# Performance work log

Measured on AMD Instinct MI355X. Metric: run time of the kernel, lower is better.

The kernel has to match this reference:

```python
import jax, jax.numpy as jnp
import numpy as np

B, S, F, H = 4, 1024, 256, 8
SCALE = float(F) ** 0.5  # source MULTIPLIES logits by sqrt(f)


def setup_inputs() -> dict:
    key = jax.random.key(0)
    ks = jax.random.split(key, 5)
    # 0.02 init scale keeps sigmoid logits in a non-saturated range
    return {
        "q_input": jax.random.normal(ks[0], (B, S, F), dtype=jnp.float32),
        "Wq": jax.random.normal(ks[1], (F, F * H), dtype=jnp.float32) * 0.02,
        "Wk": jax.random.normal(ks[2], (F, F * H), dtype=jnp.float32) * 0.02,
        "Wv": jax.random.normal(ks[3], (F, F * H), dtype=jnp.float32) * 0.02,
        "Wo": jax.random.normal(ks[4], (F * H, F), dtype=jnp.float32) * 0.02,
    }


def reference(q_input, Wq, Wk, Wv, Wo):
    b, s, f = q_input.shape
    h = Wq.shape[1] // f
    # kv_input is None in source -> self-attention (kv = q_input)
    q = (q_input.reshape(b * s, f) @ Wq).reshape(b, s, f, h)
    k = (q_input.reshape(b * s, f) @ Wk).reshape(b, s, f, h)
    v = (q_input.reshape(b * s, f) @ Wv).reshape(b, s, f, h)
    qkt = jnp.einsum('bifh,bjfh->bijh', q, k)          # [b, i, j, h]
    attn = jax.nn.sigmoid(qkt * SCALE)                  # sigmoid, NOT softmax
    wv = jnp.einsum('bijh,bjfh->bifh', attn, v)         # [b, i, f, h]
    wv = wv.reshape(b * s, f * h)
    out = jax.nn.relu(wv @ Wo)                          # projection + ReLU
    return out.reshape(b, s, f)
```

## Files before the change

### kernel.cpp

```cpp
#include <hip/hip_runtime.h>
#include <math.h>

#define SQ 1024
#define FQ 256
#define FH 2048

typedef _Float16 f16;
typedef f16  f16x8 __attribute__((ext_vector_type(8)));
typedef float f32x4 __attribute__((ext_vector_type(4)));

#define GLOAD_LDS16(gp, lp) \
    __builtin_amdgcn_global_load_lds((const __attribute__((address_space(1))) void*)(gp), \
                                     (__attribute__((address_space(3))) void*)(lp), 16, 0, 0)

#define SIG16(s) __builtin_amdgcn_rcpf(1.0f + __builtin_amdgcn_exp2f(-23.083120654223414f * (s)))

__global__ __launch_bounds__(256) void prep_kernel(const float* __restrict__ x,
                                                   const float* __restrict__ Wq,
                                                   const float* __restrict__ Wk,
                                                   const float* __restrict__ Wv,
                                                   const float* __restrict__ Wo,
                                                   f16* __restrict__ xh,
                                                   f16* __restrict__ wqT,
                                                   f16* __restrict__ wkT,
                                                   f16* __restrict__ wvT,
                                                   f16* __restrict__ woT) {
    const int z = blockIdx.z;
    if (z == 4) {
        int id = (int)(blockIdx.x * 8 + blockIdx.y);
        int idx = (id * 256 + (int)threadIdx.x) * 8;
        float4 a = *(const float4*)(x + idx);
        float4 b = *(const float4*)(x + idx + 4);
        f16x8 v = {(f16)a.x, (f16)a.y, (f16)a.z, (f16)a.w,
                   (f16)b.x, (f16)b.y, (f16)b.z, (f16)b.w};
        *(f16x8*)(xh + idx) = v;
        return;
    }
    __shared__ f16 T[32][33];
    const int tx = threadIdx.x & 31, ty = threadIdx.x >> 5;
    if (z < 3) {
        const float* W = z == 0 ? Wq : (z == 1 ? Wk : Wv);
        f16* WT        = z == 0 ? wqT : (z == 1 ? wkT : wvT);
        const int n0 = blockIdx.x * 32, k0 = blockIdx.y * 32;
#pragma unroll
        for (int i = 0; i < 4; ++i)
            T[ty + i * 8][tx] = (f16)W[(size_t)(k0 + ty + i * 8) * FH + n0 + tx];
        __syncthreads();
#pragma unroll
        for (int i = 0; i < 4; ++i)
            WT[(size_t)(n0 + ty + i * 8) * FQ + k0 + tx] = T[tx][ty + i * 8];
    } else {
        const int n0 = (blockIdx.x >> 3) * 32;
        const int yy = (blockIdx.x & 7) * 8 + blockIdx.y;
        const int ft = yy >> 3, h = yy & 7;
#pragma unroll
        for (int i = 0; i < 4; ++i) {
            int fl = ty + i * 8;
            T[fl][tx] = (f16)Wo[(size_t)((ft * 32 + fl) * 8 + h) * FQ + n0 + tx];
        }
        __syncthreads();
#pragma unroll
        for (int i = 0; i < 4; ++i)
            woT[(size_t)(n0 + ty + i * 8) * FH + h * 256 + ft * 32 + tx] = T[tx][ty + i * 8];
    }
}

__device__ __forceinline__ void stage_sw64(const f16* __restrict__ G, int ldg,
                                           int row0, int c0, f16* S,
                                           int nrows, int w, int lane) {
    const int rsub = lane >> 3;
    const int g    = (lane & 7) ^ (rsub & 7);
#pragma unroll
    for (int rI = w; rI < (nrows >> 3); rI += 4) {
        GLOAD_LDS16(G + (size_t)(row0 + rI * 8 + rsub) * ldg + c0 + g * 8,
                    S + rI * 512);
    }
}

__device__ __forceinline__ void gemm128_sw(const f16* __restrict__ A, int lda,
                                           const f16* __restrict__ Bt, int ldb,
                                           int kbeg, int kend, f16* As, f16* Bs,
                                           f32x4 acc[4][4], int row0, int col0) {
    const int t = threadIdx.x, lane = t & 63, w = t >> 6;
    const int wr = w >> 1, wc = w & 1;
    const int lrow = lane & 15, quad = lane >> 4;
    for (int k0 = kbeg; k0 < kend; k0 += 64) {
        __syncthreads();
        stage_sw64(A, lda, row0, k0, As, 128, w, lane);
        stage_sw64(Bt, ldb, col0, k0, Bs, 128, w, lane);
        __syncthreads();
#pragma unroll
        for (int kk = 0; kk < 2; ++kk) {
            f16x8 af[4], bf[4];
#pragma unroll
            for (int i = 0; i < 4; ++i) {
                int r = wr * 64 + i * 16 + lrow;
                af[i] = *(const f16x8*)&As[r * 64 + (((kk * 4 + quad) ^ (r & 7)) << 3)];
            }
#pragma unroll
            for (int j = 0; j < 4; ++j) {
                int r = wc * 64 + j * 16 + lrow;
                bf[j] = *(const f16x8*)&Bs[r * 64 + (((kk * 4 + quad) ^ (r & 7)) << 3)];
            }
#pragma unroll
            for (int i = 0; i < 4; ++i)
#pragma unroll
                for (int j = 0; j < 4; ++j)
                    acc[i][j] = __builtin_amdgcn_mfma_f32_16x16x32_f16(af[i], bf[j], acc[i][j], 0, 0, 0);
        }
    }
}

__global__ __launch_bounds__(256) void proj_mfma(const f16* __restrict__ xh,
                                                 const f16* __restrict__ wqT,
                                                 const f16* __restrict__ wkT,
                                                 const f16* __restrict__ wvT,
                                                 f16* __restrict__ qb,
                                                 f16* __restrict__ kb,
                                                 f16* __restrict__ vb) {
    const int z = blockIdx.z;
    const f16* WT = z == 0 ? wqT : (z == 1 ? wkT : wvT);
    f16* O        = z == 0 ? qb  : (z == 1 ? kb  : vb);
    __shared__ f16 smem[17408];
    f16* As = smem;
    f16* Bs = smem + 8192;
    f32x4 acc[4][4] = {};
    const int row0 = blockIdx.y * 128, col0 = blockIdx.x * 128;
    gemm128_sw(xh, FQ, WT, FQ, 0, FQ, As, Bs, acc, row0, col0);

    __syncthreads();
    f16* Es = smem;
    const int lane = threadIdx.x & 63, w = threadIdx.x >> 6;
    const int wr = w >> 1, wc = w & 1;
    const int lrow = lane & 15, quad = lane >> 4;
    if (z != 2) {
#pragma unroll
        for (int i = 0; i < 4; ++i)
#pragma unroll
            for (int rr = 0; rr < 4; ++rr) {
                int rl = 64 * wr + 16 * i + 4 * quad + rr;
#pragma unroll
                for (int j = 0; j < 4; ++j) {
                    int cc = 64 * wc + 16 * j + lrow;
                    Es[rl * 136 + (cc & 7) * 16 + (cc >> 3)] = (f16)acc[i][j][rr];
                }
            }
        __syncthreads();
        const int f0 = col0 >> 3;
#pragma unroll
        for (int it = 0; it < 4; ++it) {
            int c = it * 256 + threadIdx.x;
            int row = c >> 3, hh = c & 7;
            int gr = row0 + row, bbb = gr >> 10, s = gr & 1023;
            f16x8 v0 = *(const f16x8*)&Es[row * 136 + hh * 16];
            f16x8 v1 = *(const f16x8*)&Es[row * 136 + hh * 16 + 8];
            f16* dst = O + ((size_t)(bbb * 8 + hh) * SQ + s) * FQ + f0;
            *(f16x8*)dst = v0;
            *(f16x8*)(dst + 8) = v1;
        }
    } else {
#pragma unroll
        for (int i = 0; i < 4; ++i)
#pragma unroll
            for (int rr = 0; rr < 4; ++rr) {
                int rl = 64 * wr + 16 * i + 4 * quad + rr;
#pragma unroll
                for (int j = 0; j < 4; ++j) {
                    int cc = 64 * wc + 16 * j + lrow;
                    Es[cc * 136 + rl] = (f16)acc[i][j][rr];
                }
            }
        __syncthreads();
        const int bbb = row0 >> 10, s0 = row0 & 1023;
#pragma unroll
        for (int it = 0; it < 8; ++it) {
            int c = it * 256 + threadIdx.x;
            int cc = c >> 4, sc = c & 15;
            int hh = cc & 7, f = (col0 >> 3) + (cc >> 3);
            f16x8 v = *(const f16x8*)&Es[cc * 136 + sc * 8];
            *(f16x8*)(O + ((size_t)(bbb * 8 + hh) * FQ + f) * SQ + s0 + sc * 8) = v;
        }
    }
}

__global__ __launch_bounds__(512, 2) void fused_attn(const f16* __restrict__ Qb,
                                                     const f16* __restrict__ Kb,
                                                     const f16* __restrict__ Vt,
                                                     f16* __restrict__ WV) {
    __shared__ f16 smem[75776];
    const int t = threadIdx.x, lane = t & 63, w = t >> 6;
    const int grp = w >> 2, wl = w & 3;
    const int lrow = lane & 15, quad = lane >> 4;
    f16* Pw = smem + 65536 + w * 1280;
    const int n = blockIdx.x;
    const int xcd = n & 7, rest = n >> 3;
    const int bh = xcd * 4 + (rest & 3);
    const int strip = rest >> 2;
    const int m0 = strip * 128;
    const int bb = bh >> 3, h = bh & 7;
    const f16* Qg = Qb + (size_t)bh * SQ * FQ;
    const f16* Kg = Kb + (size_t)bh * SQ * FQ;
    const f16* Vg = Vt + (size_t)bh * FQ * SQ;

    f16x8 qf[2][8];
#pragma unroll
    for (int mi = 0; mi < 2; ++mi)
#pragma unroll
        for (int ks = 0; ks < 8; ++ks)
            qf[mi][ks] = *(const f16x8*)(Qg + (size_t)(m0 + 32 * wl + 16 * mi + lrow) * FQ
                                             + ks * 32 + quad * 8);

    const int krs = lane >> 5;
    const int kgp = lane & 31;
    const int vrs = lane >> 2;
    const int vgp = lane & 3;

    if (grp == 0) {
#pragma unroll
        for (int kt = 0; kt < 2; ++kt)
#pragma unroll
            for (int i = 0; i < 4; ++i) {
                int rI = wl + i * 4;
                int r = rI * 2 + krs;
                GLOAD_LDS16(Kg + (size_t)(kt * 32 + r) * FQ + ((kgp ^ (r & 7)) << 3),
                            smem + kt * 8192 + rI * 512);
            }
    } else {
#pragma unroll
        for (int kt = 0; kt < 2; ++kt)
#pragma unroll
            for (int i = 0; i < 4; ++i) {
                int rI = wl + i * 4;
                int f = rI * 16 + vrs;
                GLOAD_LDS16(Vg + (size_t)f * SQ + kt * 32 + ((vgp ^ ((f >> 1) & 3)) << 3),
                            smem + 32768 + kt * 8192 + rI * 512);
            }
    }

    f32x4 acc_o[2][16] = {};

    for (int it = 0; it < 16; ++it) {
        const int p = it & 1;
        f16* KBc = smem + (p * 2 + grp) * 8192;
        f16* VBc = smem + 32768 + (p * 2 + grp) * 8192;
        __syncthreads();
        if (it < 15) {
            const int pn = p ^ 1;
            const int base = (it + 1) * 64;
            if (grp == 0) {
#pragma unroll
                for (int kt = 0; kt < 2; ++kt)
#pragma unroll
                    for (int i = 0; i < 4; ++i) {
                        int rI = wl + i * 4;
                        int r = rI * 2 + krs;
                        GLOAD_LDS16(Kg + (size_t)(base + kt * 32 + r) * FQ + ((kgp ^ (r & 7)) << 3),
                                    smem + (pn * 2 + kt) * 8192 + rI * 512);
                    }
            } else {
#pragma unroll
                for (int kt = 0; kt < 2; ++kt)
#pragma unroll
                    for (int i = 0; i < 4; ++i) {
                        int rI = wl + i * 4;
                        int f = rI * 16 + vrs;
                        GLOAD_LDS16(Vg + (size_t)f * SQ + base + kt * 32 + ((vgp ^ ((f >> 1) & 3)) << 3),
                                    smem + 32768 + (pn * 2 + kt) * 8192 + rI * 512);
                    }
            }
        }
        f32x4 acc_s[2][2] = {};
#pragma unroll
        for (int ks = 0; ks < 8; ++ks) {
            f16x8 bf[2];
#pragma unroll
            for (int nj = 0; nj < 2; ++nj) {
                int rk = 16 * nj + lrow;
                bf[nj] = *(const f16x8*)&KBc[rk * 256 + (((ks * 4 + quad) ^ (rk & 7)) << 3)];
            }
#pragma unroll
            for (int mi = 0; mi < 2; ++mi)
#pragma unroll
                for (int nj = 0; nj < 2; ++nj)
                    acc_s[mi][nj] = __builtin_amdgcn_mfma_f32_16x16x32_f16(
                        qf[mi][ks], bf[nj], acc_s[mi][nj], 0, 0, 0);
        }
#pragma unroll
        for (int mi = 0; mi < 2; ++mi)
#pragma unroll
            for (int nj = 0; nj < 2; ++nj)
#pragma unroll
                for (int rr = 0; rr < 4; ++rr)
                    Pw[(16 * mi + 4 * quad + rr) * 40 + 16 * nj + lrow] =
                        (f16)SIG16(acc_s[mi][nj][rr]);
        f16x8 ap[2];
#pragma unroll
        for (int mi = 0; mi < 2; ++mi)
            ap[mi] = *(const f16x8*)&Pw[(16 * mi + lrow) * 40 + quad * 8];
#pragma unroll
        for (int nj = 0; nj < 16; ++nj) {
            int f = 16 * nj + lrow;
            f16x8 bv = *(const f16x8*)&VBc[f * 32 + ((quad ^ ((f >> 1) & 3)) << 3)];
#pragma unroll
            for (int mi = 0; mi < 2; ++mi)
                acc_o[mi][nj] = __builtin_amdgcn_mfma_f32_16x16x32_f16(
                    ap[mi], bv, acc_o[mi][nj], 0, 0, 0);
        }
    }
    __syncthreads();
    float* Fb = (float*)(smem + 34816);
    f16* Es = smem;
#pragma unroll
    for (int mi = 0; mi < 2; ++mi) {
        if (grp == 1) {
#pragma unroll
            for (int nj = 0; nj < 16; ++nj)
                *(f32x4*)&Fb[((wl * 16 + nj) << 8) + lane * 4] = acc_o[mi][nj];
        }
        __syncthreads();
        if (grp == 0) {
#pragma unroll
            for (int nj = 0; nj < 16; ++nj) {
                f32x4 s = acc_o[mi][nj] +
                          *(const f32x4*)&Fb[((wl * 16 + nj) << 8) + lane * 4];
#pragma unroll
                for (int rr = 0; rr < 4; ++rr)
                    Es[(32 * wl + 16 * mi + 4 * quad + rr) * 264 + 16 * nj + lrow] =
                        (f16)s[rr];
            }
        }
        __syncthreads();
    }
#pragma unroll
    for (int it = 0; it < 8; ++it) {
        int c = it * 512 + t;
        int r = c >> 5, ck = c & 31;
        f16x8 v = *(const f16x8*)&Es[r * 264 + ck * 8];
        *(f16x8*)(WV + (size_t)(bb * SQ + m0 + r) * FH + h * 256 + ck * 8) = v;
    }
}

__global__ __launch_bounds__(256) void out_mfma8(const f16* __restrict__ WVm,
                                                 const f16* __restrict__ WoT,
                                                 float* __restrict__ PP) {
    __shared__ f16 smem[16384];
    f16* As = smem;
    f16* Bs = smem + 8192;
    f32x4 acc[4][4] = {};
    const int row0 = blockIdx.y * 128, col0 = blockIdx.x * 128;
    const int kbeg = blockIdx.z * 256;
    gemm128_sw(WVm, FH, WoT, FH, kbeg, kbeg + 256, As, Bs, acc, row0, col0);

    float* P = PP + (size_t)blockIdx.z * SQ * 4 * FQ;
    const int lane = threadIdx.x & 63, w = threadIdx.x >> 6;
    const int wr = w >> 1, wc = w & 1;
    const int lrow = lane & 15, quad = lane >> 4;
#pragma unroll
    for (int i = 0; i < 4; ++i)
#pragma unroll
        for (int rr = 0; rr < 4; ++rr) {
            int gr = row0 + wr * 64 + i * 16 + quad * 4 + rr;
#pragma unroll
            for (int j = 0; j < 4; ++j) {
                int gc = col0 + wc * 64 + j * 16 + lrow;
                P[(size_t)gr * FQ + gc] = acc[i][j][rr];
            }
        }
}

__global__ __launch_bounds__(256) void reduce_relu8(const float* __restrict__ PP,
                                                    float* __restrict__ O) {
    int idx = (blockIdx.x * 256 + threadIdx.x) * 4;
    f32x4 s = *(const f32x4*)(PP + idx);
#pragma unroll
    for (int z = 1; z < 8; ++z)
        s += *(const f32x4*)(PP + (size_t)z * 1048576 + idx);
    f32x4 r = {fmaxf(s.x, 0.f), fmaxf(s.y, 0.f), fmaxf(s.z, 0.f), fmaxf(s.w, 0.f)};
    *(f32x4*)(O + idx) = r;
}

extern "C" void kernel_launch(void* const* d_in, const int* in_sizes, int n_in,
                              void* d_out, int out_size, void* d_ws, size_t ws_size,
                              hipStream_t stream) {
    const float* x  = (const float*)d_in[0];
    const float* Wq = (const float*)d_in[1];
    const float* Wk = (const float*)d_in[2];
    const float* Wv = (const float*)d_in[3];
    const float* Wo = (const float*)d_in[4];
    float* out = (float*)d_out;

    f16* ws = (f16*)d_ws;
    f16* xh    = ws;
    f16* wqT   = xh    + 1048576;
    f16* wkT   = wqT   + 524288;
    f16* wvT   = wkT   + 524288;
    f16* woT   = wvT   + 524288;
    f16* qbuf  = woT   + 524288;
    f16* kbuf  = qbuf  + 8388608;
    f16* vbuf  = kbuf  + 8388608;
    f16* wvbuf = vbuf  + 8388608;
    float* pp  = (float*)qbuf;

    dim3 blk(256);
    prep_kernel<<<dim3(64, 8, 5), blk, 0, stream>>>(x, Wq, Wk, Wv, Wo,
                                                    xh, wqT, wkT, wvT, woT);

    proj_mfma<<<dim3(16, 32, 3), blk, 0, stream>>>(xh, wqT, wkT, wvT, qbuf, kbuf, vbuf);

    fused_attn<<<dim3(256), dim3(512), 0, stream>>>(qbuf, kbuf, vbuf, wvbuf);

    out_mfma8<<<dim3(2, 32, 8), blk, 0, stream>>>(wvbuf, woT, pp);
    reduce_relu8<<<dim3(1024), blk, 0, stream>>>(pp, out);
}
```

Measured before the change: 161.3 us.

## Keep sigmoid probabilities in registers via transposed QK^T MFMA layout

Swaps the MFMA operand order for the QK^T product so the score accumulator lands in the layout needed as the A operand of the PV product. This removes the per-warp LDS write/read round trip for the sigmoid probabilities. The PV product now uses 16x16x16 MFMAs with 4-wide V fragments, which doubles the MFMA instruction count and the number of V reads from LDS. It also raises wave priority with s_setprio around the PV loop.

Result: slower. 176.2 us (+9.2%).

```diff
diff --git a/kernel.cpp b/kernel.cpp
--- a/kernel.cpp
+++ b/kernel.cpp
@@ -7,6 +7,7 @@
 
 typedef _Float16 f16;
 typedef f16  f16x8 __attribute__((ext_vector_type(8)));
+typedef f16  f16x4 __attribute__((ext_vector_type(4)));
 typedef float f32x4 __attribute__((ext_vector_type(4)));
 
 #define GLOAD_LDS16(gp, lp) \
@@ -191,7 +192,6 @@
     const int t = threadIdx.x, lane = t & 63, w = t >> 6;
     const int grp = w >> 2, wl = w & 3;
     const int lrow = lane & 15, quad = lane >> 4;
-    f16* Pw = smem + 65536 + w * 1280;
     const int n = blockIdx.x;
     const int xcd = n & 7, rest = n >> 3;
     const int bh = xcd * 4 + (rest & 3);
@@ -279,33 +279,39 @@
                 bf[nj] = *(const f16x8*)&KBc[rk * 256 + (((ks * 4 + quad) ^ (rk & 7)) << 3)];
             }
 #pragma unroll
-            for (int mi = 0; mi < 2; ++mi)
-#pragma unroll
-                for (int nj = 0; nj < 2; ++nj)
-                    acc_s[mi][nj] = __builtin_amdgcn_mfma_f32_16x16x32_f16(
-                        qf[mi][ks], bf[nj], acc_s[mi][nj], 0, 0, 0);
-        }
-#pragma unroll
-        for (int mi = 0; mi < 2; ++mi)
-#pragma unroll
             for (int nj = 0; nj < 2; ++nj)
 #pragma unroll
+                for (int mi = 0; mi < 2; ++mi)
+                    acc_s[nj][mi] = __builtin_amdgcn_mfma_f32_16x16x32_f16(
+                        bf[nj], qf[mi][ks], acc_s[nj][mi], 0, 0, 0);
+        }
+        f16x4 ap[2][2];
+#pragma unroll
+        for (int nj = 0; nj < 2; ++nj)
+#pragma unroll
+            for (int mi = 0; mi < 2; ++mi) {
+                f16x4 v;
+#pragma unroll
                 for (int rr = 0; rr < 4; ++rr)
-                    Pw[(16 * mi + 4 * quad + rr) * 40 + 16 * nj + lrow] =
-                        (f16)SIG16(acc_s[mi][nj][rr]);
-        f16x8 ap[2];
-#pragma unroll
-        for (int mi = 0; mi < 2; ++mi)
-            ap[mi] = *(const f16x8*)&Pw[(16 * mi + lrow) * 40 + quad * 8];
-#pragma unroll
-        for (int nj = 0; nj < 16; ++nj) {
-            int f = 16 * nj + lrow;
-            f16x8 bv = *(const f16x8*)&VBc[f * 32 + ((quad ^ ((f >> 1) & 3)) << 3)];
-#pragma unroll
-            for (int mi = 0; mi < 2; ++mi)
-                acc_o[mi][nj] = __builtin_amdgcn_mfma_f32_16x16x32_f16(
-                    ap[mi], bv, acc_o[mi][nj], 0, 0, 0);
-        }
+                    v[rr] = (f16)SIG16(acc_s[nj][mi][rr]);
+                ap[nj][mi] = v;
+            }
+        __builtin_amdgcn_s_setprio(1);
+#pragma unroll
+        for (int njf = 0; njf < 16; ++njf) {
+            const int f = 16 * njf + lrow;
+            const int sw = (f >> 1) & 3;
+#pragma unroll
+            for (int nj = 0; nj < 2; ++nj) {
+                const int g16 = 2 * nj + (quad >> 1);
+                f16x4 bv = *(const f16x4*)&VBc[f * 32 + ((g16 ^ sw) << 3) + ((quad & 1) << 2)];
+#pragma unroll
+                for (int mi = 0; mi < 2; ++mi)
+                    acc_o[mi][njf] = __builtin_amdgcn_mfma_f32_16x16x16f16(
+                        ap[nj][mi], bv, acc_o[mi][njf], 0, 0, 0);
+            }
+        }
+        __builtin_amdgcn_s_setprio(0);
     }
     __syncthreads();
     float* Fb = (float*)(smem + 34816);
```
